# Kernel optimization log

Measured on AMD Instinct MI355X. Metric: run time of the kernel, lower is better.

Reference implementation:

```python
import jax, jax.numpy as jnp
import numpy as np

WS = (8, 8)          # window size
NHEAD = 6
D_MODEL = 192

def _rel_pos_index(ws):
    coords = np.stack(np.meshgrid(np.arange(ws[0]), np.arange(ws[1]), indexing='ij'))  # (2, wh, ww)
    cf = coords.reshape(2, -1)                          # (2, N)
    rel = cf[:, :, None] - cf[:, None, :]               # (2, N, N)
    rel = rel.transpose(1, 2, 0).astype(np.int64)       # (N, N, 2)
    rel[:, :, 0] += ws[0] - 1
    rel[:, :, 1] += ws[1] - 1
    rel[:, :, 0] *= 2 * ws[1] - 1
    return rel.sum(-1)                                  # (N, N)

REL_IDX = jnp.asarray(_rel_pos_index(WS))

def setup_inputs() -> dict:
    key = jax.random.key(0)
    ks = jax.random.split(key, 6)
    B, H, W, C = 4, 256, 256, D_MODEL
    x = jax.random.normal(ks[0], (B, H * W, C), dtype=jnp.float32)
    qkv_w = jax.random.normal(ks[1], (3 * C, C), dtype=jnp.float32) * 0.02
    qkv_b = jnp.zeros((3 * C,), dtype=jnp.float32)
    proj_w = jax.random.normal(ks[2], (C, C), dtype=jnp.float32) * 0.02
    proj_b = jnp.zeros((C,), dtype=jnp.float32)
    n_bias = (2 * WS[0] - 1) * (2 * WS[1] - 1)
    rpb_table = jax.random.normal(ks[3], (n_bias, NHEAD), dtype=jnp.float32) * 0.02
    return {"x": x, "qkv_w": qkv_w, "qkv_b": qkv_b, "proj_w": proj_w,
            "proj_b": proj_b, "rpb_table": rpb_table, "H": H, "W": W}

def reference(x, qkv_w, qkv_b, proj_w, proj_b, rpb_table, H, W):
    B, Ni, C = x.shape
    h, d = NHEAD, C // NHEAD
    wh, ww = WS
    nH, nW = H // wh, W // ww
    N = wh * ww
    # window partition: (B, H, W, C) -> (B*nH*nW, N, C)
    xw = x.reshape(B, nH, wh, nW, ww, C).transpose(0, 1, 3, 2, 4, 5).reshape(-1, N, C)
    qkv = xw @ qkv_w.T + qkv_b                           # (B_, N, 3C)
    B_ = xw.shape[0]
    qkv = qkv.reshape(B_, N, 3, h, d).transpose(2, 0, 3, 1, 4)  # (3, B_, h, N, d)
    q, k, v = qkv[0], qkv[1], qkv[2]
    scale = d ** -0.5
    attn = jnp.einsum('bhnd,bhmd->bhnm', q, k) * scale   # (B_, h, N, N)
    bias = rpb_table[REL_IDX.reshape(-1)].reshape(N, N, h).transpose(2, 0, 1)  # (h, N, N)
    attn = jax.nn.softmax(attn + bias[None], axis=-1)
    out = jnp.einsum('bhnm,bhmd->bhnd', attn, v)         # (B_, h, N, d)
    out = out.transpose(0, 2, 1, 3).reshape(B_, N, C)
    out = out @ proj_w.T + proj_b
    # window reverse: (B*nH*nW, N, C) -> (B, H*W, C)
    out = out.reshape(B, nH, nW, wh, ww, C).transpose(0, 1, 3, 2, 4, 5).reshape(B, Ni, C)
    return out
```

## Files before the change

kernel.cpp:

```cpp
#include <hip/hip_runtime.h>

#define CDIM 192
#define NHEAD 6

typedef __bf16 bf16x8 __attribute__((ext_vector_type(8)));
typedef float f32x4 __attribute__((ext_vector_type(4)));
typedef unsigned int u32x4 __attribute__((ext_vector_type(4)));

#define X_OFF  0
#define Q_OFF  25600
#define K_OFF  51200
#define VT_OFF 76800
#define BI_OFF 104448
#define SMEM_BYTES 153600
#define XS  200
#define QS  200
#define KS  200
#define VTS 72
#define AOS 200
#define PS  72
#define OFS 196
#define SCALE 0.17677669529663687f

__device__ __forceinline__ unsigned short f2b(float f) {
    unsigned int u = __float_as_uint(f);
    u = (u + 0x7FFFu + ((u >> 16) & 1u)) >> 16;
    return (unsigned short)u;
}
__device__ __forceinline__ float b2f(unsigned short h) {
    return __uint_as_float(((unsigned int)h) << 16);
}

#define WS_W1   0
#define WS_W2   221184
#define WS_BIAS 294912

__global__ void prep(const float* __restrict__ qkv_w, const float* __restrict__ proj_w,
                     const float* __restrict__ rpb,
                     unsigned short* __restrict__ W1, unsigned short* __restrict__ W2,
                     unsigned short* __restrict__ BIAS) {
    int t = blockIdx.x * 256 + threadIdx.x;
    if (t < 110592) { W1[t] = f2b(qkv_w[t]); return; }
    t -= 110592;
    if (t < 36864)  { W2[t] = f2b(proj_w[t]); return; }
    t -= 36864;
    {
        int h = t >> 12, ij = t & 4095;
        int i = ij >> 6, j = ij & 63;
        int idx = ((i >> 3) - (j >> 3) + 7) * 15 + ((i & 7) - (j & 7) + 7);
        BIAS[t] = f2b(rpb[idx * NHEAD + h]);
    }
}

__global__ __launch_bounds__(512, 2)
void win_attn(const float* __restrict__ x,
              const unsigned short* __restrict__ qkv_w,
              const float* __restrict__ qkv_b,
              const unsigned short* __restrict__ proj_w,
              const float* __restrict__ proj_b,
              const unsigned short* __restrict__ biasg,
              float* __restrict__ out)
{
    extern __shared__ __align__(16) char smem[];
    __bf16* xl  = (__bf16*)(smem + X_OFF);
    __bf16* ql  = (__bf16*)(smem + Q_OFF);
    __bf16* kl  = (__bf16*)(smem + K_OFF);
    __bf16* vt  = (__bf16*)(smem + VT_OFF);
    unsigned short* biasL = (unsigned short*)(smem + BI_OFF);
    __bf16* aob = (__bf16*)(smem + K_OFF);
    float* stagef = (float*)(smem);

    const int tid  = threadIdx.x;
    const int wv   = tid >> 6;
    const int lane = tid & 63;
    const int l15  = lane & 15;
    const int g    = lane >> 4;
    const int g4   = g << 2;
    const int g8   = g << 3;

    const int wid = blockIdx.x;
    const int b   = wid >> 10;
    const int wy  = (wid >> 5) & 31;
    const int wx  = wid & 31;
    const long long base0 = (long long)(b * 65536 + wy * 8 * 256 + wx * 8) * CDIM;

    #pragma unroll
    for (int r = 0; r < 6; ++r) {
        int i = tid + r * 512;
        int t = i / 48, part = i - t * 48;
        int iy = t >> 3, ix = t & 7;
        f32x4 v = *(const f32x4*)(x + base0 + (iy * 256 + ix) * CDIM + part * 4);
        __bf16* dst = xl + t * XS + part * 4;
        dst[0] = (__bf16)v[0]; dst[1] = (__bf16)v[1];
        dst[2] = (__bf16)v[2]; dst[3] = (__bf16)v[3];
    }
    #pragma unroll
    for (int r = 0; r < 6; ++r) {
        int i = tid + r * 512;
        *(u32x4*)(biasL + i * 8) = *(const u32x4*)(biasg + i * 8);
    }
    __syncthreads();

    {
        const int qstart_lut[8] = {0, 5, 10, 15, 20, 25, 30, 31};
        const int start = qstart_lut[wv];

        f32x4 acc[4][5];
        #pragma unroll
        for (int mt = 0; mt < 4; ++mt)
            #pragma unroll
            for (int jn = 0; jn < 5; ++jn)
                acc[mt][jn] = (f32x4){0.f, 0.f, 0.f, 0.f};

        #pragma unroll
        for (int kk = 0; kk < 6; ++kk) {
            bf16x8 aa[4];
            #pragma unroll
            for (int mt = 0; mt < 4; ++mt)
                aa[mt] = *(const bf16x8*)(xl + (mt * 16 + l15) * XS + kk * 32 + g8);
            #pragma unroll
            for (int jn = 0; jn < 5; ++jn) {
                int o = (start + jn) * 16 + l15;
                bf16x8 bw = *(const bf16x8*)((const __bf16*)qkv_w + o * CDIM + kk * 32 + g8);
                #pragma unroll
                for (int mt = 0; mt < 4; ++mt)
                    acc[mt][jn] = __builtin_amdgcn_mfma_f32_16x16x32_bf16(aa[mt], bw, acc[mt][jn], 0, 0, 0);
            }
        }
        #pragma unroll
        for (int jn = 0; jn < 5; ++jn) {
            int nt = start + jn;
            int o  = nt * 16 + l15;
            float qb = qkv_b[o];
            #pragma unroll
            for (int mt = 0; mt < 4; ++mt) {
                #pragma unroll
                for (int rr = 0; rr < 4; ++rr) {
                    int tr = mt * 16 + g4 + rr;
                    float val = acc[mt][jn][rr] + qb;
                    if (nt < 12)       ql[tr * QS + o] = (__bf16)val;
                    else if (nt < 24)  kl[tr * KS + (o - 192)] = (__bf16)val;
                    else               vt[(o - 384) * VTS + tr] = (__bf16)val;
                }
            }
        }
    }
    __syncthreads();

    f32x4 sh[3][4];
    #pragma unroll
    for (int u = 0; u < 3; ++u) {
        int gu = wv * 3 + u;
        int hu = gu >> 2;
        int rb = gu & 3;

        bf16x8 aq = *(const bf16x8*)(ql + (rb * 16 + l15) * QS + hu * 32 + g8);
        #pragma unroll
        for (int ni = 0; ni < 4; ++ni) {
            bf16x8 bk = *(const bf16x8*)(kl + (ni * 16 + l15) * KS + hu * 32 + g8);
            sh[u][ni] = __builtin_amdgcn_mfma_f32_16x16x32_bf16(aq, bk, (f32x4){0.f, 0.f, 0.f, 0.f}, 0, 0, 0);
        }

        const unsigned short* brow = biasL + hu * 4096;
        #pragma unroll
        for (int rr = 0; rr < 4; ++rr) {
            int row = rb * 16 + g4 + rr;
            float v0 = sh[u][0][rr] * SCALE + b2f(brow[row * 64 +  0 + l15]);
            float v1 = sh[u][1][rr] * SCALE + b2f(brow[row * 64 + 16 + l15]);
            float v2 = sh[u][2][rr] * SCALE + b2f(brow[row * 64 + 32 + l15]);
            float v3 = sh[u][3][rr] * SCALE + b2f(brow[row * 64 + 48 + l15]);
            float m = fmaxf(fmaxf(v0, v1), fmaxf(v2, v3));
            m = fmaxf(m, __shfl_xor(m, 1));
            m = fmaxf(m, __shfl_xor(m, 2));
            m = fmaxf(m, __shfl_xor(m, 4));
            m = fmaxf(m, __shfl_xor(m, 8));
            v0 = __expf(v0 - m); v1 = __expf(v1 - m);
            v2 = __expf(v2 - m); v3 = __expf(v3 - m);
            float s = v0 + v1 + v2 + v3;
            s += __shfl_xor(s, 1); s += __shfl_xor(s, 2);
            s += __shfl_xor(s, 4); s += __shfl_xor(s, 8);
            float inv = 1.0f / s;
            sh[u][0][rr] = v0 * inv;
            sh[u][1][rr] = v1 * inv;
            sh[u][2][rr] = v2 * inv;
            sh[u][3][rr] = v3 * inv;
        }
    }
    __syncthreads();

    #pragma unroll
    for (int u = 0; u < 3; ++u) {
        int gu = wv * 3 + u;
        int hu = gu >> 2;
        int rb = gu & 3;
        __bf16* ph = (__bf16*)(smem + X_OFF) + wv * (16 * PS);

        #pragma unroll
        for (int rr = 0; rr < 4; ++rr) {
            int pr = (g4 + rr) * PS;
            ph[pr +  0 + l15] = (__bf16)sh[u][0][rr];
            ph[pr + 16 + l15] = (__bf16)sh[u][1][rr];
            ph[pr + 32 + l15] = (__bf16)sh[u][2][rr];
            ph[pr + 48 + l15] = (__bf16)sh[u][3][rr];
        }
        __threadfence_block();

        f32x4 oacc[2];
        oacc[0] = (f32x4){0.f, 0.f, 0.f, 0.f};
        oacc[1] = (f32x4){0.f, 0.f, 0.f, 0.f};
        #pragma unroll
        for (int kk = 0; kk < 2; ++kk) {
            bf16x8 pa = *(const bf16x8*)(ph + l15 * PS + kk * 32 + g8);
            #pragma unroll
            for (int nj = 0; nj < 2; ++nj) {
                bf16x8 bv = *(const bf16x8*)(vt + (hu * 32 + nj * 16 + l15) * VTS + kk * 32 + g8);
                oacc[nj] = __builtin_amdgcn_mfma_f32_16x16x32_bf16(pa, bv, oacc[nj], 0, 0, 0);
            }
        }
        __threadfence_block();
        #pragma unroll
        for (int nj = 0; nj < 2; ++nj)
            #pragma unroll
            for (int rr = 0; rr < 4; ++rr)
                aob[(rb * 16 + g4 + rr) * AOS + hu * 32 + nj * 16 + l15] = (__bf16)oacc[nj][rr];
    }
    __syncthreads();

    {
        const int pstart_lut[8] = {0, 2, 4, 6, 8, 10, 10, 10};
        const int start = pstart_lut[wv];

        f32x4 pacc[4][2];
        #pragma unroll
        for (int mt = 0; mt < 4; ++mt)
            #pragma unroll
            for (int jn = 0; jn < 2; ++jn)
                pacc[mt][jn] = (f32x4){0.f, 0.f, 0.f, 0.f};

        #pragma unroll
        for (int kk = 0; kk < 6; ++kk) {
            bf16x8 aa[4];
            #pragma unroll
            for (int mt = 0; mt < 4; ++mt)
                aa[mt] = *(const bf16x8*)(aob + (mt * 16 + l15) * AOS + kk * 32 + g8);
            #pragma unroll
            for (int jn = 0; jn < 2; ++jn) {
                int o = (start + jn) * 16 + l15;
                bf16x8 bw = *(const bf16x8*)((const __bf16*)proj_w + o * CDIM + kk * 32 + g8);
                #pragma unroll
                for (int mt = 0; mt < 4; ++mt)
                    pacc[mt][jn] = __builtin_amdgcn_mfma_f32_16x16x32_bf16(aa[mt], bw, pacc[mt][jn], 0, 0, 0);
            }
        }
        __syncthreads();
        #pragma unroll
        for (int jn = 0; jn < 2; ++jn) {
            int o = (start + jn) * 16 + l15;
            float pb = proj_b[o];
            #pragma unroll
            for (int mt = 0; mt < 4; ++mt)
                #pragma unroll
                for (int rr = 0; rr < 4; ++rr) {
                    int tr = mt * 16 + g4 + rr;
                    stagef[tr * OFS + o] = pacc[mt][jn][rr] + pb;
                }
        }
    }
    __syncthreads();

    #pragma unroll
    for (int r = 0; r < 6; ++r) {
        int i = tid + r * 512;
        int t = i / 48, part = i - t * 48;
        int iy = t >> 3, ix = t & 7;
        *(f32x4*)(out + base0 + (iy * 256 + ix) * CDIM + part * 4) =
            *(const f32x4*)(stagef + t * OFS + part * 4);
    }
}

extern "C" void kernel_launch(void* const* d_in, const int* in_sizes, int n_in,
                              void* d_out, int out_size, void* d_ws, size_t ws_size,
                              hipStream_t stream) {
    const float* x      = (const float*)d_in[0];
    const float* qkv_w  = (const float*)d_in[1];
    const float* qkv_b  = (const float*)d_in[2];
    const float* proj_w = (const float*)d_in[3];
    const float* proj_b = (const float*)d_in[4];
    const float* rpb    = (const float*)d_in[5];
    float* outp = (float*)d_out;

    char* ws = (char*)d_ws;
    unsigned short* W1 = (unsigned short*)(ws + WS_W1);
    unsigned short* W2 = (unsigned short*)(ws + WS_W2);
    unsigned short* BIAS = (unsigned short*)(ws + WS_BIAS);

    hipFuncSetAttribute((const void*)win_attn,
                        hipFuncAttributeMaxDynamicSharedMemorySize, SMEM_BYTES);

    prep<<<672, 256, 0, stream>>>(qkv_w, proj_w, rpb, W1, W2, BIAS);
    win_attn<<<4096, 512, SMEM_BYTES, stream>>>(x, W1, qkv_b, W2, proj_b, BIAS, outp);
}
```

Baseline: 406.8 us.

## Shrink window-attention block to 256 threads and cut LDS footprint

After: 400.5 us. Within noise of the previous version (-1.6%).

```diff
diff --git a/kernel.cpp b/kernel.cpp
--- a/kernel.cpp
+++ b/kernel.cpp
@@ -5,14 +5,11 @@
 
 typedef __bf16 bf16x8 __attribute__((ext_vector_type(8)));
 typedef float f32x4 __attribute__((ext_vector_type(4)));
-typedef unsigned int u32x4 __attribute__((ext_vector_type(4)));
-
-#define X_OFF  0
-#define Q_OFF  25600
-#define K_OFF  51200
-#define VT_OFF 76800
-#define BI_OFF 104448
-#define SMEM_BYTES 153600
+
+#define Q_OFF  0
+#define K_OFF  25600
+#define VT_OFF 51200
+#define SMEM_BYTES 78848
 #define XS  200
 #define QS  200
 #define KS  200
@@ -27,9 +24,6 @@
     u = (u + 0x7FFFu + ((u >> 16) & 1u)) >> 16;
     return (unsigned short)u;
 }
-__device__ __forceinline__ float b2f(unsigned short h) {
-    return __uint_as_float(((unsigned int)h) << 16);
-}
 
 #define WS_W1   0
 #define WS_W2   221184
@@ -38,7 +32,7 @@
 __global__ void prep(const float* __restrict__ qkv_w, const float* __restrict__ proj_w,
                      const float* __restrict__ rpb,
                      unsigned short* __restrict__ W1, unsigned short* __restrict__ W2,
-                     unsigned short* __restrict__ BIAS) {
+                     float* __restrict__ BIAS) {
     int t = blockIdx.x * 256 + threadIdx.x;
     if (t < 110592) { W1[t] = f2b(qkv_w[t]); return; }
     t -= 110592;
@@ -48,25 +42,24 @@
         int h = t >> 12, ij = t & 4095;
         int i = ij >> 6, j = ij & 63;
         int idx = ((i >> 3) - (j >> 3) + 7) * 15 + ((i & 7) - (j & 7) + 7);
-        BIAS[t] = f2b(rpb[idx * NHEAD + h]);
-    }
-}
-
-__global__ __launch_bounds__(512, 2)
+        BIAS[t] = rpb[idx * NHEAD + h];
+    }
+}
+
+__global__ __launch_bounds__(256, 2)
 void win_attn(const float* __restrict__ x,
               const unsigned short* __restrict__ qkv_w,
               const float* __restrict__ qkv_b,
               const unsigned short* __restrict__ proj_w,
               const float* __restrict__ proj_b,
-              const unsigned short* __restrict__ biasg,
+              const float* __restrict__ bias,
               float* __restrict__ out)
 {
     extern __shared__ __align__(16) char smem[];
-    __bf16* xl  = (__bf16*)(smem + X_OFF);
     __bf16* ql  = (__bf16*)(smem + Q_OFF);
     __bf16* kl  = (__bf16*)(smem + K_OFF);
     __bf16* vt  = (__bf16*)(smem + VT_OFF);
-    unsigned short* biasL = (unsigned short*)(smem + BI_OFF);
+    __bf16* xk  = (__bf16*)(smem + K_OFF);
     __bf16* aob = (__bf16*)(smem + K_OFF);
     float* stagef = (float*)(smem);
 
@@ -85,31 +78,25 @@
     const long long base0 = (long long)(b * 65536 + wy * 8 * 256 + wx * 8) * CDIM;
 
     #pragma unroll
-    for (int r = 0; r < 6; ++r) {
-        int i = tid + r * 512;
+    for (int r = 0; r < 12; ++r) {
+        int i = tid + r * 256;
         int t = i / 48, part = i - t * 48;
         int iy = t >> 3, ix = t & 7;
         f32x4 v = *(const f32x4*)(x + base0 + (iy * 256 + ix) * CDIM + part * 4);
-        __bf16* dst = xl + t * XS + part * 4;
+        __bf16* dst = xk + t * XS + part * 4;
         dst[0] = (__bf16)v[0]; dst[1] = (__bf16)v[1];
         dst[2] = (__bf16)v[2]; dst[3] = (__bf16)v[3];
     }
-    #pragma unroll
-    for (int r = 0; r < 6; ++r) {
-        int i = tid + r * 512;
-        *(u32x4*)(biasL + i * 8) = *(const u32x4*)(biasg + i * 8);
-    }
     __syncthreads();
 
     {
-        const int qstart_lut[8] = {0, 5, 10, 15, 20, 25, 30, 31};
-        const int start = qstart_lut[wv];
-
-        f32x4 acc[4][5];
+        const int start = wv * 9;
+
+        f32x4 acc[4][9];
         #pragma unroll
         for (int mt = 0; mt < 4; ++mt)
             #pragma unroll
-            for (int jn = 0; jn < 5; ++jn)
+            for (int jn = 0; jn < 9; ++jn)
                 acc[mt][jn] = (f32x4){0.f, 0.f, 0.f, 0.f};
 
         #pragma unroll
@@ -117,9 +104,9 @@
             bf16x8 aa[4];
             #pragma unroll
             for (int mt = 0; mt < 4; ++mt)
-                aa[mt] = *(const bf16x8*)(xl + (mt * 16 + l15) * XS + kk * 32 + g8);
-            #pragma unroll
-            for (int jn = 0; jn < 5; ++jn) {
+                aa[mt] = *(const bf16x8*)(xk + (mt * 16 + l15) * XS + kk * 32 + g8);
+            #pragma unroll
+            for (int jn = 0; jn < 9; ++jn) {
                 int o = (start + jn) * 16 + l15;
                 bf16x8 bw = *(const bf16x8*)((const __bf16*)qkv_w + o * CDIM + kk * 32 + g8);
                 #pragma unroll
@@ -127,8 +114,10 @@
                     acc[mt][jn] = __builtin_amdgcn_mfma_f32_16x16x32_bf16(aa[mt], bw, acc[mt][jn], 0, 0, 0);
             }
         }
-        #pragma unroll
-        for (int jn = 0; jn < 5; ++jn) {
+        __syncthreads();
+
+        #pragma unroll
+        for (int jn = 0; jn < 9; ++jn) {
             int nt = start + jn;
             int o  = nt * 16 + l15;
             float qb = qkv_b[o];
@@ -147,10 +136,10 @@
     }
     __syncthreads();
 
-    f32x4 sh[3][4];
-    #pragma unroll
-    for (int u = 0; u < 3; ++u) {
-        int gu = wv * 3 + u;
+    f32x4 sh[6][4];
+    #pragma unroll
+    for (int u = 0; u < 6; ++u) {
+        int gu = wv * 6 + u;
         int hu = gu >> 2;
         int rb = gu & 3;
 
@@ -161,14 +150,14 @@
             sh[u][ni] = __builtin_amdgcn_mfma_f32_16x16x32_bf16(aq, bk, (f32x4){0.f, 0.f, 0.f, 0.f}, 0, 0, 0);
         }
 
-        const unsigned short* brow = biasL + hu * 4096;
+        const float* brow = bias + hu * 4096;
         #pragma unroll
         for (int rr = 0; rr < 4; ++rr) {
             int row = rb * 16 + g4 + rr;
-            float v0 = sh[u][0][rr] * SCALE + b2f(brow[row * 64 +  0 + l15]);
-            float v1 = sh[u][1][rr] * SCALE + b2f(brow[row * 64 + 16 + l15]);
-            float v2 = sh[u][2][rr] * SCALE + b2f(brow[row * 64 + 32 + l15]);
-            float v3 = sh[u][3][rr] * SCALE + b2f(brow[row * 64 + 48 + l15]);
+            float v0 = sh[u][0][rr] * SCALE + brow[row * 64 +  0 + l15];
+            float v1 = sh[u][1][rr] * SCALE + brow[row * 64 + 16 + l15];
+            float v2 = sh[u][2][rr] * SCALE + brow[row * 64 + 32 + l15];
+            float v3 = sh[u][3][rr] * SCALE + brow[row * 64 + 48 + l15];
             float m = fmaxf(fmaxf(v0, v1), fmaxf(v2, v3));
             m = fmaxf(m, __shfl_xor(m, 1));
             m = fmaxf(m, __shfl_xor(m, 2));
@@ -189,11 +178,11 @@
     __syncthreads();
 
     #pragma unroll
-    for (int u = 0; u < 3; ++u) {
-        int gu = wv * 3 + u;
+    for (int u = 0; u < 6; ++u) {
+        int gu = wv * 6 + u;
         int hu = gu >> 2;
         int rb = gu & 3;
-        __bf16* ph = (__bf16*)(smem + X_OFF) + wv * (16 * PS);
+        __bf16* ph = (__bf16*)(smem + Q_OFF) + wv * (16 * PS);
 
         #pragma unroll
         for (int rr = 0; rr < 4; ++rr) {
@@ -227,14 +216,13 @@
     __syncthreads();
 
     {
-        const int pstart_lut[8] = {0, 2, 4, 6, 8, 10, 10, 10};
-        const int start = pstart_lut[wv];
-
-        f32x4 pacc[4][2];
+        const int start = wv * 3;
+
+        f32x4 pacc[4][3];
         #pragma unroll
         for (int mt = 0; mt < 4; ++mt)
             #pragma unroll
-            for (int jn = 0; jn < 2; ++jn)
+            for (int jn = 0; jn < 3; ++jn)
                 pacc[mt][jn] = (f32x4){0.f, 0.f, 0.f, 0.f};
 
         #pragma unroll
@@ -244,7 +232,7 @@
             for (int mt = 0; mt < 4; ++mt)
                 aa[mt] = *(const bf16x8*)(aob + (mt * 16 + l15) * AOS + kk * 32 + g8);
             #pragma unroll
-            for (int jn = 0; jn < 2; ++jn) {
+            for (int jn = 0; jn < 3; ++jn) {
                 int o = (start + jn) * 16 + l15;
                 bf16x8 bw = *(const bf16x8*)((const __bf16*)proj_w + o * CDIM + kk * 32 + g8);
                 #pragma unroll
@@ -254,7 +242,7 @@
         }
         __syncthreads();
         #pragma unroll
-        for (int jn = 0; jn < 2; ++jn) {
+        for (int jn = 0; jn < 3; ++jn) {
             int o = (start + jn) * 16 + l15;
             float pb = proj_b[o];
             #pragma unroll
@@ -269,8 +257,8 @@
     __syncthreads();
 
     #pragma unroll
-    for (int r = 0; r < 6; ++r) {
-        int i = tid + r * 512;
+    for (int r = 0; r < 12; ++r) {
+        int i = tid + r * 256;
         int t = i / 48, part = i - t * 48;
         int iy = t >> 3, ix = t & 7;
         *(f32x4*)(out + base0 + (iy * 256 + ix) * CDIM + part * 4) =
@@ -292,11 +280,11 @@
     char* ws = (char*)d_ws;
     unsigned short* W1 = (unsigned short*)(ws + WS_W1);
     unsigned short* W2 = (unsigned short*)(ws + WS_W2);
-    unsigned short* BIAS = (unsigned short*)(ws + WS_BIAS);
+    float* BIAS = (float*)(ws + WS_BIAS);
 
     hipFuncSetAttribute((const void*)win_attn,
                         hipFuncAttributeMaxDynamicSharedMemorySize, SMEM_BYTES);
 
     prep<<<672, 256, 0, stream>>>(qkv_w, proj_w, rpb, W1, W2, BIAS);
-    win_attn<<<4096, 512, SMEM_BYTES, stream>>>(x, W1, qkv_b, W2, proj_b, BIAS, outp);
-}
+    win_attn<<<4096, 256, SMEM_BYTES, stream>>>(x, W1, qkv_b, W2, proj_b, BIAS, outp);
+}
```
